# Kernel optimization log

Hardware: AMD Instinct MI355X
Metric: run time of the kernel (lower is better)

The kernel has to match this reference:

```python
import jax, jax.numpy as jnp
import numpy as np


def _cdist(a, b):
    # Euclidean pairwise distances, [N, M]
    d2 = (jnp.sum(a * a, axis=1)[:, None]
          + jnp.sum(b * b, axis=1)[None, :]
          - 2.0 * (a @ b.T))
    return jnp.sqrt(jnp.maximum(d2, 0.0))


def setup_inputs() -> dict:
    key = jax.random.key(0)
    k1, k2 = jax.random.split(key)
    N, M, D = 12288, 12288, 3
    true_pos = jax.random.normal(k1, (N, D), dtype=jnp.float32)
    pred_pos = jax.random.normal(k2, (M, D), dtype=jnp.float32)
    return {"true_pos": true_pos, "pred_pos": pred_pos}


def reference(true_pos, pred_pos):
    dists = _cdist(true_pos.astype(jnp.float32), pred_pos.astype(jnp.float32))
    mins = jnp.min(dists, axis=1)        # per true point -> nearest pred
    mins_seeds = jnp.min(dists, axis=0)  # per pred point -> nearest true
    loss = jnp.mean(mins)
    loss_seeds = jnp.mean(mins_seeds)
    just_in_case_losses = (loss, loss_seeds)
    # use_loss=True branch
    return (loss + loss_seeds, mins_seeds, just_in_case_losses)
```

## Files before the change

### kernel.cpp

```cpp
#include <hip/hip_runtime.h>
#include <cfloat>

typedef __bf16 bf16x8 __attribute__((ext_vector_type(8)));
typedef unsigned short ushort8 __attribute__((ext_vector_type(8)));
typedef float f32x16 __attribute__((ext_vector_type(16)));

#define S_SLICES 4

static __device__ __forceinline__ unsigned short f2bf(float x) {
    unsigned u = __float_as_uint(x);
    return (unsigned short)((u + 0x7FFFu + ((u >> 16) & 1u)) >> 16);
}
static __device__ __forceinline__ float bfbits2f(unsigned short h) {
    return __uint_as_float(((unsigned)h) << 16);
}

__global__ __launch_bounds__(256) void prep_kernel(
    const float* __restrict__ A, const float* __restrict__ B,
    ushort8* __restrict__ RFA, ushort8* __restrict__ CFA,
    ushort8* __restrict__ RFB, ushort8* __restrict__ CFB,
    float* __restrict__ hdr, int n, int m, int RTn, int RTm)
{
    const int i = blockIdx.x * 256 + threadIdx.x;
    if (i < 8) hdr[i] = 0.f;
    const unsigned short one = 0x3F80;

#pragma unroll
    for (int side = 0; side < 2; ++side) {
        const int cntPts = side ? RTm * 32 : RTn * 32;
        if (i >= cntPts) continue;
        const float* P = side ? B : A;
        const int lim = side ? m : n;
        ushort8* RF = side ? RFB : RFA;
        ushort8* CF = side ? CFB : CFA;

        float x = 0.f, y = 0.f, z = 0.f, nrm = 1e30f;
        if (i < lim) { x = P[3*i]; y = P[3*i+1]; z = P[3*i+2];
                       nrm = fmaf(x, x, fmaf(y, y, z * z)); }
        const unsigned short hx = f2bf(x), hy = f2bf(y), hz = f2bf(z);
        const unsigned short lx = f2bf(x - bfbits2f(hx)),
                             ly = f2bf(y - bfbits2f(hy)),
                             lz = f2bf(z - bfbits2f(hz));
        const unsigned short nhx = f2bf(-2.f * bfbits2f(hx)),
                             nhy = f2bf(-2.f * bfbits2f(hy)),
                             nhz = f2bf(-2.f * bfbits2f(hz));
        const unsigned short nlx = f2bf(-2.f * bfbits2f(lx)),
                             nly = f2bf(-2.f * bfbits2f(ly)),
                             nlz = f2bf(-2.f * bfbits2f(lz));
        float r = nrm;
        const unsigned short s1 = f2bf(r); r -= bfbits2f(s1);
        const unsigned short s2 = f2bf(r); r -= bfbits2f(s2);
        const unsigned short s3 = f2bf(r);

        const int t = i >> 5, l5 = i & 31;
        ushort8 rq0 = { nhx, nhy, nhz, nhx, nhy, nhz, nlx, nly };
        ushort8 rq1 = { nlz, s1, s2, s3, one, one, one, 0 };
        RF[t * 64 + l5]      = rq0;
        RF[t * 64 + 32 + l5] = rq1;
        ushort8 cq0 = { hx, hy, hz, lx, ly, lz, hx, hy };
        ushort8 cq1 = { hz, one, one, one, s1, s2, s3, 0 };
        CF[t * 64 + l5]      = cq0;
        CF[t * 64 + 32 + l5] = cq1;
    }
}

#define MINC(C)                                             \
    _Pragma("unroll")                                       \
    for (int r = 0; r < 16; ++r) macc[r] = fminf(macc[r], (C)[r]);

__global__ __launch_bounds__(256, 4) void pairmin_kernel(
    const bf16x8* __restrict__ RFA, const bf16x8* __restrict__ CFA,
    const bf16x8* __restrict__ RFB, const bf16x8* __restrict__ CFB,
    float* __restrict__ sbuf, int RTn, int RTm)
{
    const int lane = threadIdx.x & 63;
    const int wave = threadIdx.x >> 6;

    const bf16x8* RF; const bf16x8* CF; float* sb; int rtCount, ctCount, stride;
    if (blockIdx.z == 0) { RF = RFA; CF = CFB; rtCount = RTn; ctCount = RTm;
                           sb = sbuf; stride = RTn * 32; }
    else                 { RF = RFB; CF = CFA; rtCount = RTm; ctCount = RTn;
                           sb = sbuf + (size_t)S_SLICES * RTn * 32;
                           stride = RTm * 32; }

    const int rt = blockIdx.x * 4 + wave;
    if (rt >= rtCount) return;
    sb += (size_t)blockIdx.y * stride;

    const int ctPer = (ctCount + S_SLICES - 1) / S_SLICES;
    const int ctBeg = min(blockIdx.y * ctPer, ctCount);
    const int ctEnd = min(ctBeg + ctPer, ctCount);

    const bf16x8 afrag = RF[rt * 64 + lane];
    const f32x16 zc = {};

    float macc[16];
#pragma unroll
    for (int r = 0; r < 16; ++r) macc[r] = FLT_MAX;

    if (ctBeg < ctEnd) {
        int ct = ctBeg;
        const int last = ctEnd - 1;
        bf16x8 q0 = CF[(size_t)ct * 64 + lane];
        bf16x8 q1 = CF[(size_t)min(ct + 1, last) * 64 + lane];
        bf16x8 q2 = CF[(size_t)min(ct + 2, last) * 64 + lane];
        bf16x8 q3 = CF[(size_t)min(ct + 3, last) * 64 + lane];
        f32x16 C0 = __builtin_amdgcn_mfma_f32_32x32x16_bf16(afrag, q0, zc, 0, 0, 0);
        f32x16 C1 = __builtin_amdgcn_mfma_f32_32x32x16_bf16(afrag, q1, zc, 0, 0, 0);

        for (; ct + 7 < ctEnd; ct += 4) {
            q0 = CF[(size_t)(ct + 4) * 64 + lane];
            MINC(C0);
            C0 = __builtin_amdgcn_mfma_f32_32x32x16_bf16(afrag, q2, zc, 0, 0, 0);
            q1 = CF[(size_t)(ct + 5) * 64 + lane];
            MINC(C1);
            C1 = __builtin_amdgcn_mfma_f32_32x32x16_bf16(afrag, q3, zc, 0, 0, 0);
            q2 = CF[(size_t)(ct + 6) * 64 + lane];
            MINC(C0);
            C0 = __builtin_amdgcn_mfma_f32_32x32x16_bf16(afrag, q0, zc, 0, 0, 0);
            q3 = CF[(size_t)(ct + 7) * 64 + lane];
            MINC(C1);
            C1 = __builtin_amdgcn_mfma_f32_32x32x16_bf16(afrag, q1, zc, 0, 0, 0);
        }
        MINC(C0);
        MINC(C1);
        if (ct + 2 < ctEnd) {
            const f32x16 C =
                __builtin_amdgcn_mfma_f32_32x32x16_bf16(afrag, q2, zc, 0, 0, 0);
            MINC(C);
        }
        if (ct + 3 < ctEnd) {
            const f32x16 C =
                __builtin_amdgcn_mfma_f32_32x32x16_bf16(afrag, q3, zc, 0, 0, 0);
            MINC(C);
        }
        for (int t = ct + 4; t < ctEnd; ++t) {
            const bf16x8 b = CF[(size_t)t * 64 + lane];
            const f32x16 C =
                __builtin_amdgcn_mfma_f32_32x32x16_bf16(afrag, b, zc, 0, 0, 0);
            MINC(C);
        }
    }

#pragma unroll
    for (int r = 0; r < 16; ++r) {
        float v = macc[r];
        v = fminf(v, __shfl_xor(v, 1, 64));
        v = fminf(v, __shfl_xor(v, 2, 64));
        v = fminf(v, __shfl_xor(v, 4, 64));
        v = fminf(v, __shfl_xor(v, 8, 64));
        v = fminf(v, __shfl_xor(v, 16, 64));
        macc[r] = v;
    }
    if ((lane & 31) == 0) {
        const int q4 = (lane >> 5) * 4;
        float* dst = sb + rt * 32;
#pragma unroll
        for (int r = 0; r < 16; ++r)
            dst[(r & 3) + 8 * (r >> 2) + q4] = macc[r];
    }
}

__global__ __launch_bounds__(256) void finalize_kernel(
    const float* __restrict__ sbuf, float* __restrict__ hdr,
    float* __restrict__ out, int n, int m, int RTn, int RTm)
{
    const int i = blockIdx.x * 256 + threadIdx.x;
    const int strideA = RTn * 32, strideB = RTm * 32;
    const float* sbB = sbuf + (size_t)S_SLICES * strideA;

    float sa = 0.f, sb_ = 0.f;
    if (i < n) {
        float s = FLT_MAX;
#pragma unroll
        for (int k = 0; k < S_SLICES; ++k) s = fminf(s, sbuf[(size_t)k * strideA + i]);
        sa = sqrtf(fmaxf(s, 0.f));
    }
    if (i < m) {
        float s = FLT_MAX;
#pragma unroll
        for (int k = 0; k < S_SLICES; ++k) s = fminf(s, sbB[(size_t)k * strideB + i]);
        const float v = sqrtf(fmaxf(s, 0.f));
        out[1 + i] = v;
        sb_ = v;
    }

#pragma unroll
    for (int off = 32; off > 0; off >>= 1) {
        sa  += __shfl_down(sa,  off, 64);
        sb_ += __shfl_down(sb_, off, 64);
    }
    __shared__ float reda[4], redb[4];
    const int wave = threadIdx.x >> 6;
    const int lane = threadIdx.x & 63;
    if (lane == 0) { reda[wave] = sa; redb[wave] = sb_; }
    __syncthreads();

    if (threadIdx.x == 0) {
        const float ta = reda[0] + reda[1] + reda[2] + reda[3];
        const float tb = redb[0] + redb[1] + redb[2] + redb[3];
        atomicAdd(&hdr[0], ta);
        atomicAdd(&hdr[1], tb);
        __threadfence();
        const unsigned ticket = atomicAdd((unsigned*)&hdr[2], 1u);
        if (ticket == (unsigned)(gridDim.x - 1)) {
            const float fa = atomicAdd(&hdr[0], 0.f);
            const float fb = atomicAdd(&hdr[1], 0.f);
            const float loss = fa / (float)n;
            const float loss_seeds = fb / (float)m;
            out[0] = loss + loss_seeds;
            out[1 + m] = loss;
            out[2 + m] = loss_seeds;
        }
    }
}

extern "C" void kernel_launch(void* const* d_in, const int* in_sizes, int n_in,
                              void* d_out, int out_size, void* d_ws, size_t ws_size,
                              hipStream_t stream) {
    const int n = in_sizes[0] / 3;
    const int m = in_sizes[1] / 3;
    const float* A = (const float*)d_in[0];
    const float* B = (const float*)d_in[1];
    float* out = (float*)d_out;

    const int RTn = (n + 31) / 32, RTm = (m + 31) / 32;
    char* p = (char*)d_ws;
    float*   hdr  = (float*)p;    p += 64;
    float*   sbuf = (float*)p;    p += (size_t)S_SLICES * (RTn + RTm) * 32 * 4;
    ushort8* RFA  = (ushort8*)p;  p += (size_t)RTn * 64 * 16;
    ushort8* CFA  = (ushort8*)p;  p += (size_t)RTn * 64 * 16;
    ushort8* RFB  = (ushort8*)p;  p += (size_t)RTm * 64 * 16;
    ushort8* CFB  = (ushort8*)p;

    const int maxPts = ((RTn > RTm) ? RTn : RTm) * 32;
    prep_kernel<<<(maxPts + 255) / 256, 256, 0, stream>>>(
        A, B, RFA, CFA, RFB, CFB, hdr, n, m, RTn, RTm);

    const int maxRT = (RTn > RTm) ? RTn : RTm;
    dim3 grid((maxRT + 3) / 4, S_SLICES, 2);
    pairmin_kernel<<<grid, 256, 0, stream>>>(
        (const bf16x8*)RFA, (const bf16x8*)CFA,
        (const bf16x8*)RFB, (const bf16x8*)CFB, sbuf, RTn, RTm);

    const int maxnm = (n > m) ? n : m;
    finalize_kernel<<<(maxnm + 255) / 256, 256, 0, stream>>>(
        sbuf, hdr, out, n, m, RTn, RTm);
}
```

Before: 78.16 us.

## Fuse finalize into pairmin via per-row-tile last-slice ticket reduction

Removes the separate finalize kernel. Each wave bumps a per-row-tile atomic counter after writing its partial minima, and the last of the S_SLICES waves to arrive combines the slices, takes the sqrt, writes the outputs and adds to the global sums. A global ticket then lets the final tile write the loss scalars. This saves one kernel launch and an extra pass over sbuf, in exchange for extra atomics and threadfences in every wave plus counter zeroing in prep.

New measurement: 138.9 us. 1.78x slower.

```diff
diff --git a/kernel.cpp b/kernel.cpp
--- a/kernel.cpp
+++ b/kernel.cpp
@@ -19,10 +19,13 @@
     const float* __restrict__ A, const float* __restrict__ B,
     ushort8* __restrict__ RFA, ushort8* __restrict__ CFA,
     ushort8* __restrict__ RFB, ushort8* __restrict__ CFB,
-    float* __restrict__ hdr, int n, int m, int RTn, int RTm)
+    float* __restrict__ hdr, unsigned* __restrict__ rtc,
+    int n, int m, int RTn, int RTm)
 {
     const int i = blockIdx.x * 256 + threadIdx.x;
     if (i < 8) hdr[i] = 0.f;
+    const int maxRT = (RTn > RTm) ? RTn : RTm;
+    if (i < 2 * maxRT) rtc[i] = 0u;
     const unsigned short one = 0x3F80;
 
 #pragma unroll
@@ -71,21 +74,25 @@
 __global__ __launch_bounds__(256, 4) void pairmin_kernel(
     const bf16x8* __restrict__ RFA, const bf16x8* __restrict__ CFA,
     const bf16x8* __restrict__ RFB, const bf16x8* __restrict__ CFB,
-    float* __restrict__ sbuf, int RTn, int RTm)
+    float* __restrict__ sbuf, unsigned* __restrict__ rtc,
+    float* __restrict__ hdr, float* __restrict__ out,
+    int n, int m, int RTn, int RTm)
 {
     const int lane = threadIdx.x & 63;
     const int wave = threadIdx.x >> 6;
-
-    const bf16x8* RF; const bf16x8* CF; float* sb; int rtCount, ctCount, stride;
+    const int maxRT = (RTn > RTm) ? RTn : RTm;
+
+    const bf16x8* RF; const bf16x8* CF; float* sb0;
+    int rtCount, ctCount, stride, lim;
     if (blockIdx.z == 0) { RF = RFA; CF = CFB; rtCount = RTn; ctCount = RTm;
-                           sb = sbuf; stride = RTn * 32; }
+                           sb0 = sbuf; stride = RTn * 32; lim = n; }
     else                 { RF = RFB; CF = CFA; rtCount = RTm; ctCount = RTn;
-                           sb = sbuf + (size_t)S_SLICES * RTn * 32;
-                           stride = RTm * 32; }
+                           sb0 = sbuf + (size_t)S_SLICES * RTn * 32;
+                           stride = RTm * 32; lim = m; }
 
     const int rt = blockIdx.x * 4 + wave;
     if (rt >= rtCount) return;
-    sb += (size_t)blockIdx.y * stride;
+    float* sby = sb0 + (size_t)blockIdx.y * stride;
 
     const int ctPer = (ctCount + S_SLICES - 1) / S_SLICES;
     const int ctBeg = min(blockIdx.y * ctPer, ctCount);
@@ -154,63 +161,47 @@
     }
     if ((lane & 31) == 0) {
         const int q4 = (lane >> 5) * 4;
-        float* dst = sb + rt * 32;
+        float* dst = sby + rt * 32;
 #pragma unroll
         for (int r = 0; r < 16; ++r)
             dst[(r & 3) + 8 * (r >> 2) + q4] = macc[r];
     }
-}
-
-__global__ __launch_bounds__(256) void finalize_kernel(
-    const float* __restrict__ sbuf, float* __restrict__ hdr,
-    float* __restrict__ out, int n, int m, int RTn, int RTm)
-{
-    const int i = blockIdx.x * 256 + threadIdx.x;
-    const int strideA = RTn * 32, strideB = RTm * 32;
-    const float* sbB = sbuf + (size_t)S_SLICES * strideA;
-
-    float sa = 0.f, sb_ = 0.f;
-    if (i < n) {
-        float s = FLT_MAX;
-#pragma unroll
-        for (int k = 0; k < S_SLICES; ++k) s = fminf(s, sbuf[(size_t)k * strideA + i]);
-        sa = sqrtf(fmaxf(s, 0.f));
-    }
-    if (i < m) {
-        float s = FLT_MAX;
-#pragma unroll
-        for (int k = 0; k < S_SLICES; ++k) s = fminf(s, sbB[(size_t)k * strideB + i]);
-        const float v = sqrtf(fmaxf(s, 0.f));
-        out[1 + i] = v;
-        sb_ = v;
-    }
-
-#pragma unroll
-    for (int off = 32; off > 0; off >>= 1) {
-        sa  += __shfl_down(sa,  off, 64);
-        sb_ += __shfl_down(sb_, off, 64);
-    }
-    __shared__ float reda[4], redb[4];
-    const int wave = threadIdx.x >> 6;
-    const int lane = threadIdx.x & 63;
-    if (lane == 0) { reda[wave] = sa; redb[wave] = sb_; }
-    __syncthreads();
-
-    if (threadIdx.x == 0) {
-        const float ta = reda[0] + reda[1] + reda[2] + reda[3];
-        const float tb = redb[0] + redb[1] + redb[2] + redb[3];
-        atomicAdd(&hdr[0], ta);
-        atomicAdd(&hdr[1], tb);
+
+    unsigned tk = 0u;
+    if (lane == 0) {
         __threadfence();
-        const unsigned ticket = atomicAdd((unsigned*)&hdr[2], 1u);
-        if (ticket == (unsigned)(gridDim.x - 1)) {
-            const float fa = atomicAdd(&hdr[0], 0.f);
-            const float fb = atomicAdd(&hdr[1], 0.f);
-            const float loss = fa / (float)n;
-            const float loss_seeds = fb / (float)m;
-            out[0] = loss + loss_seeds;
-            out[1 + m] = loss;
-            out[2 + m] = loss_seeds;
+        tk = atomicAdd(&rtc[blockIdx.z * maxRT + rt], 1u);
+    }
+    tk = __shfl(tk, 0, 64);
+    if (tk == S_SLICES - 1) {
+        const int idx = rt * 32 + (lane & 31);
+        float d = 0.f;
+        if (lane < 32) {
+            float s = FLT_MAX;
+#pragma unroll
+            for (int k = 0; k < S_SLICES; ++k)
+                s = fminf(s, sb0[(size_t)k * stride + idx]);
+            if (idx < lim) {
+                d = sqrtf(fmaxf(s, 0.f));
+                if (blockIdx.z == 1) out[1 + idx] = d;
+            }
+        }
+#pragma unroll
+        for (int off = 32; off > 0; off >>= 1)
+            d += __shfl_down(d, off, 64);
+        if (lane == 0) {
+            atomicAdd(&hdr[blockIdx.z], d);
+            __threadfence();
+            const unsigned g = atomicAdd((unsigned*)&hdr[2], 1u);
+            if (g == (unsigned)(RTn + RTm - 1)) {
+                const float fa = atomicAdd(&hdr[0], 0.f);
+                const float fb = atomicAdd(&hdr[1], 0.f);
+                const float loss = fa / (float)n;
+                const float loss_seeds = fb / (float)m;
+                out[0] = loss + loss_seeds;
+                out[1 + m] = loss;
+                out[2 + m] = loss_seeds;
+            }
         }
     }
 }
@@ -225,25 +216,23 @@
     float* out = (float*)d_out;
 
     const int RTn = (n + 31) / 32, RTm = (m + 31) / 32;
+    const int maxRT = (RTn > RTm) ? RTn : RTm;
     char* p = (char*)d_ws;
-    float*   hdr  = (float*)p;    p += 64;
-    float*   sbuf = (float*)p;    p += (size_t)S_SLICES * (RTn + RTm) * 32 * 4;
-    ushort8* RFA  = (ushort8*)p;  p += (size_t)RTn * 64 * 16;
-    ushort8* CFA  = (ushort8*)p;  p += (size_t)RTn * 64 * 16;
-    ushort8* RFB  = (ushort8*)p;  p += (size_t)RTm * 64 * 16;
-    ushort8* CFB  = (ushort8*)p;
-
-    const int maxPts = ((RTn > RTm) ? RTn : RTm) * 32;
+    float*    hdr  = (float*)p;    p += 64;
+    unsigned* rtc  = (unsigned*)p; p += (((size_t)2 * maxRT * 4 + 63) / 64) * 64;
+    float*    sbuf = (float*)p;    p += (size_t)S_SLICES * (RTn + RTm) * 32 * 4;
+    ushort8*  RFA  = (ushort8*)p;  p += (size_t)RTn * 64 * 16;
+    ushort8*  CFA  = (ushort8*)p;  p += (size_t)RTn * 64 * 16;
+    ushort8*  RFB  = (ushort8*)p;  p += (size_t)RTm * 64 * 16;
+    ushort8*  CFB  = (ushort8*)p;
+
+    const int maxPts = maxRT * 32;
     prep_kernel<<<(maxPts + 255) / 256, 256, 0, stream>>>(
-        A, B, RFA, CFA, RFB, CFB, hdr, n, m, RTn, RTm);
-
-    const int maxRT = (RTn > RTm) ? RTn : RTm;
+        A, B, RFA, CFA, RFB, CFB, hdr, rtc, n, m, RTn, RTm);
+
     dim3 grid((maxRT + 3) / 4, S_SLICES, 2);
     pairmin_kernel<<<grid, 256, 0, stream>>>(
         (const bf16x8*)RFA, (const bf16x8*)CFA,
-        (const bf16x8*)RFB, (const bf16x8*)CFB, sbuf, RTn, RTm);
-
-    const int maxnm = (n > m) ? n : m;
-    finalize_kernel<<<(maxnm + 255) / 256, 256, 0, stream>>>(
-        sbuf, hdr, out, n, m, RTn, RTm);
-}
+        (const bf16x8*)RFB, (const bf16x8*)CFB,
+        sbuf, rtc, hdr, out, n, m, RTn, RTm);
+}
```

## Process two row tiles per wave to reuse column fragments and double slices

Applied to the files above, without the earlier changes.

Each wave now computes two 32-row tiles against every loaded column fragment, so each global load of CF feeds two MFMAs, halving column-fragment traffic per output. Min reduction is fused as a three-way fminf across two column tiles. To keep enough waves in flight after halving the row-wave count, the column dimension is split into 8 slices instead of 4, and launch bounds are relaxed to 3 blocks per CU to accommodate doubled accumulator registers. Risks include register pressure, lower occupancy and more partial results for finalize to combine.

Result: slower. 87.50 us (+11.9%).

```diff
diff --git a/kernel.cpp b/kernel.cpp
--- a/kernel.cpp
+++ b/kernel.cpp
@@ -5,7 +5,7 @@
 typedef unsigned short ushort8 __attribute__((ext_vector_type(8)));
 typedef float f32x16 __attribute__((ext_vector_type(16)));
 
-#define S_SLICES 4
+#define S_SLICES 8
 
 static __device__ __forceinline__ unsigned short f2bf(float x) {
     unsigned u = __float_as_uint(x);
@@ -64,11 +64,15 @@
     }
 }
 
-#define MINC(C)                                             \
+#define MINC(M, C)                                          \
     _Pragma("unroll")                                       \
-    for (int r = 0; r < 16; ++r) macc[r] = fminf(macc[r], (C)[r]);
-
-__global__ __launch_bounds__(256, 4) void pairmin_kernel(
+    for (int r = 0; r < 16; ++r) M[r] = fminf(M[r], (C)[r]);
+#define MIN3(M, Ca, Cb)                                     \
+    _Pragma("unroll")                                       \
+    for (int r = 0; r < 16; ++r)                            \
+        M[r] = fminf(M[r], fminf((Ca)[r], (Cb)[r]));
+
+__global__ __launch_bounds__(256, 3) void pairmin_kernel(
     const bf16x8* __restrict__ RFA, const bf16x8* __restrict__ CFA,
     const bf16x8* __restrict__ RFB, const bf16x8* __restrict__ CFB,
     float* __restrict__ sbuf, int RTn, int RTm)
@@ -83,20 +87,24 @@
                            sb = sbuf + (size_t)S_SLICES * RTn * 32;
                            stride = RTm * 32; }
 
-    const int rt = blockIdx.x * 4 + wave;
-    if (rt >= rtCount) return;
+    const int pairCount = (rtCount + 1) >> 1;
+    const int g = blockIdx.x * 4 + wave;
+    if (g >= pairCount) return;
+    const int rt0 = g * 2;
+    const int rt1 = min(rt0 + 1, rtCount - 1);
     sb += (size_t)blockIdx.y * stride;
 
     const int ctPer = (ctCount + S_SLICES - 1) / S_SLICES;
-    const int ctBeg = min(blockIdx.y * ctPer, ctCount);
+    const int ctBeg = min((int)blockIdx.y * ctPer, ctCount);
     const int ctEnd = min(ctBeg + ctPer, ctCount);
 
-    const bf16x8 afrag = RF[rt * 64 + lane];
+    const bf16x8 a0 = RF[rt0 * 64 + lane];
+    const bf16x8 a1 = RF[rt1 * 64 + lane];
     const f32x16 zc = {};
 
-    float macc[16];
-#pragma unroll
-    for (int r = 0; r < 16; ++r) macc[r] = FLT_MAX;
+    float macc0[16], macc1[16];
+#pragma unroll
+    for (int r = 0; r < 16; ++r) { macc0[r] = FLT_MAX; macc1[r] = FLT_MAX; }
 
     if (ctBeg < ctEnd) {
         int ct = ctBeg;
@@ -105,59 +113,83 @@
         bf16x8 q1 = CF[(size_t)min(ct + 1, last) * 64 + lane];
         bf16x8 q2 = CF[(size_t)min(ct + 2, last) * 64 + lane];
         bf16x8 q3 = CF[(size_t)min(ct + 3, last) * 64 + lane];
-        f32x16 C0 = __builtin_amdgcn_mfma_f32_32x32x16_bf16(afrag, q0, zc, 0, 0, 0);
-        f32x16 C1 = __builtin_amdgcn_mfma_f32_32x32x16_bf16(afrag, q1, zc, 0, 0, 0);
+        f32x16 C00 = __builtin_amdgcn_mfma_f32_32x32x16_bf16(a0, q0, zc, 0, 0, 0);
+        f32x16 C10 = __builtin_amdgcn_mfma_f32_32x32x16_bf16(a1, q0, zc, 0, 0, 0);
+        f32x16 C01 = __builtin_amdgcn_mfma_f32_32x32x16_bf16(a0, q1, zc, 0, 0, 0);
+        f32x16 C11 = __builtin_amdgcn_mfma_f32_32x32x16_bf16(a1, q1, zc, 0, 0, 0);
 
         for (; ct + 7 < ctEnd; ct += 4) {
             q0 = CF[(size_t)(ct + 4) * 64 + lane];
-            MINC(C0);
-            C0 = __builtin_amdgcn_mfma_f32_32x32x16_bf16(afrag, q2, zc, 0, 0, 0);
             q1 = CF[(size_t)(ct + 5) * 64 + lane];
-            MINC(C1);
-            C1 = __builtin_amdgcn_mfma_f32_32x32x16_bf16(afrag, q3, zc, 0, 0, 0);
+            MIN3(macc0, C00, C01);
+            MIN3(macc1, C10, C11);
+            C00 = __builtin_amdgcn_mfma_f32_32x32x16_bf16(a0, q2, zc, 0, 0, 0);
+            C10 = __builtin_amdgcn_mfma_f32_32x32x16_bf16(a1, q2, zc, 0, 0, 0);
+            C01 = __builtin_amdgcn_mfma_f32_32x32x16_bf16(a0, q3, zc, 0, 0, 0);
+            C11 = __builtin_amdgcn_mfma_f32_32x32x16_bf16(a1, q3, zc, 0, 0, 0);
             q2 = CF[(size_t)(ct + 6) * 64 + lane];
-            MINC(C0);
-            C0 = __builtin_amdgcn_mfma_f32_32x32x16_bf16(afrag, q0, zc, 0, 0, 0);
             q3 = CF[(size_t)(ct + 7) * 64 + lane];
-            MINC(C1);
-            C1 = __builtin_amdgcn_mfma_f32_32x32x16_bf16(afrag, q1, zc, 0, 0, 0);
-        }
-        MINC(C0);
-        MINC(C1);
+            MIN3(macc0, C00, C01);
+            MIN3(macc1, C10, C11);
+            C00 = __builtin_amdgcn_mfma_f32_32x32x16_bf16(a0, q0, zc, 0, 0, 0);
+            C10 = __builtin_amdgcn_mfma_f32_32x32x16_bf16(a1, q0, zc, 0, 0, 0);
+            C01 = __builtin_amdgcn_mfma_f32_32x32x16_bf16(a0, q1, zc, 0, 0, 0);
+            C11 = __builtin_amdgcn_mfma_f32_32x32x16_bf16(a1, q1, zc, 0, 0, 0);
+        }
+        MIN3(macc0, C00, C01);
+        MIN3(macc1, C10, C11);
         if (ct + 2 < ctEnd) {
-            const f32x16 C =
-                __builtin_amdgcn_mfma_f32_32x32x16_bf16(afrag, q2, zc, 0, 0, 0);
-            MINC(C);
+            const f32x16 c0 =
+                __builtin_amdgcn_mfma_f32_32x32x16_bf16(a0, q2, zc, 0, 0, 0);
+            const f32x16 c1 =
+                __builtin_amdgcn_mfma_f32_32x32x16_bf16(a1, q2, zc, 0, 0, 0);
+            MINC(macc0, c0);
+            MINC(macc1, c1);
         }
         if (ct + 3 < ctEnd) {
-            const f32x16 C =
-                __builtin_amdgcn_mfma_f32_32x32x16_bf16(afrag, q3, zc, 0, 0, 0);
-            MINC(C);
+            const f32x16 c0 =
+                __builtin_amdgcn_mfma_f32_32x32x16_bf16(a0, q3, zc, 0, 0, 0);
+            const f32x16 c1 =
+                __builtin_amdgcn_mfma_f32_32x32x16_bf16(a1, q3, zc, 0, 0, 0);
+            MINC(macc0, c0);
+            MINC(macc1, c1);
         }
         for (int t = ct + 4; t < ctEnd; ++t) {
             const bf16x8 b = CF[(size_t)t * 64 + lane];
-            const f32x16 C =
-                __builtin_amdgcn_mfma_f32_32x32x16_bf16(afrag, b, zc, 0, 0, 0);
-            MINC(C);
+            const f32x16 c0 =
+                __builtin_amdgcn_mfma_f32_32x32x16_bf16(a0, b, zc, 0, 0, 0);
+            const f32x16 c1 =
+                __builtin_amdgcn_mfma_f32_32x32x16_bf16(a1, b, zc, 0, 0, 0);
+            MINC(macc0, c0);
+            MINC(macc1, c1);
         }
     }
 
 #pragma unroll
     for (int r = 0; r < 16; ++r) {
-        float v = macc[r];
-        v = fminf(v, __shfl_xor(v, 1, 64));
-        v = fminf(v, __shfl_xor(v, 2, 64));
-        v = fminf(v, __shfl_xor(v, 4, 64));
-        v = fminf(v, __shfl_xor(v, 8, 64));
-        v = fminf(v, __shfl_xor(v, 16, 64));
-        macc[r] = v;
+        float v0 = macc0[r], v1 = macc1[r];
+        v0 = fminf(v0, __shfl_xor(v0, 1, 64));
+        v1 = fminf(v1, __shfl_xor(v1, 1, 64));
+        v0 = fminf(v0, __shfl_xor(v0, 2, 64));
+        v1 = fminf(v1, __shfl_xor(v1, 2, 64));
+        v0 = fminf(v0, __shfl_xor(v0, 4, 64));
+        v1 = fminf(v1, __shfl_xor(v1, 4, 64));
+        v0 = fminf(v0, __shfl_xor(v0, 8, 64));
+        v1 = fminf(v1, __shfl_xor(v1, 8, 64));
+        v0 = fminf(v0, __shfl_xor(v0, 16, 64));
+        v1 = fminf(v1, __shfl_xor(v1, 16, 64));
+        macc0[r] = v0;
+        macc1[r] = v1;
     }
     if ((lane & 31) == 0) {
         const int q4 = (lane >> 5) * 4;
-        float* dst = sb + rt * 32;
-#pragma unroll
-        for (int r = 0; r < 16; ++r)
-            dst[(r & 3) + 8 * (r >> 2) + q4] = macc[r];
+        float* dst0 = sb + rt0 * 32;
+        float* dst1 = sb + rt1 * 32;
+#pragma unroll
+        for (int r = 0; r < 16; ++r) {
+            dst0[(r & 3) + 8 * (r >> 2) + q4] = macc0[r];
+            dst1[(r & 3) + 8 * (r >> 2) + q4] = macc1[r];
+        }
     }
 }
 
@@ -233,12 +265,13 @@
     ushort8* RFB  = (ushort8*)p;  p += (size_t)RTm * 64 * 16;
     ushort8* CFB  = (ushort8*)p;
 
-    const int maxPts = ((RTn > RTm) ? RTn : RTm) * 32;
+    const int maxRT = (RTn > RTm) ? RTn : RTm;
+    const int maxPts = maxRT * 32;
     prep_kernel<<<(maxPts + 255) / 256, 256, 0, stream>>>(
         A, B, RFA, CFA, RFB, CFB, hdr, n, m, RTn, RTm);
 
-    const int maxRT = (RTn > RTm) ? RTn : RTm;
-    dim3 grid((maxRT + 3) / 4, S_SLICES, 2);
+    const int maxPair = (maxRT + 1) >> 1;
+    dim3 grid((maxPair + 3) / 4, S_SLICES, 2);
     pairmin_kernel<<<grid, 256, 0, stream>>>(
         (const bf16x8*)RFA, (const bf16x8*)CFA,
         (const bf16x8*)RFB, (const bf16x8*)CFB, sbuf, RTn, RTm);
```

## Stage column fragments in LDS via global_load_lds shared across waves

Applied to the files above, without the earlier changes.

Each block now cooperatively copies chunks of 48 column tiles into shared memory with direct global-to-LDS loads, and all four waves read their B fragments from LDS instead of each wave loading them separately from global memory. The aim is to cut redundant global/L2 traffic, since all four waves in a block use the same column tiles. The inner loop is also reordered to issue MFMA pairs and fold two results per min pass. Occupancy is lowered to 3 blocks per SM and block-wide barriers are added, and out-of-range waves now stay alive to join the barriers.

Result: slower. 86.55 us (+10.7%).

```diff
diff --git a/kernel.cpp b/kernel.cpp
--- a/kernel.cpp
+++ b/kernel.cpp
@@ -6,6 +6,7 @@
 typedef float f32x16 __attribute__((ext_vector_type(16)));
 
 #define S_SLICES 4
+#define CHUNK_T 48
 
 static __device__ __forceinline__ unsigned short f2bf(float x) {
     unsigned u = __float_as_uint(x);
@@ -67,8 +68,12 @@
 #define MINC(C)                                             \
     _Pragma("unroll")                                       \
     for (int r = 0; r < 16; ++r) macc[r] = fminf(macc[r], (C)[r]);
-
-__global__ __launch_bounds__(256, 4) void pairmin_kernel(
+#define MIN3(Ca, Cb)                                        \
+    _Pragma("unroll")                                       \
+    for (int r = 0; r < 16; ++r)                            \
+        macc[r] = fminf(macc[r], fminf((Ca)[r], (Cb)[r]));
+
+__global__ __launch_bounds__(256, 3) void pairmin_kernel(
     const bf16x8* __restrict__ RFA, const bf16x8* __restrict__ CFA,
     const bf16x8* __restrict__ RFB, const bf16x8* __restrict__ CFB,
     float* __restrict__ sbuf, int RTn, int RTm)
@@ -84,58 +89,72 @@
                            stride = RTm * 32; }
 
     const int rt = blockIdx.x * 4 + wave;
-    if (rt >= rtCount) return;
+    const bool live = rt < rtCount;
+    const int rtc = live ? rt : rtCount - 1;
     sb += (size_t)blockIdx.y * stride;
 
     const int ctPer = (ctCount + S_SLICES - 1) / S_SLICES;
-    const int ctBeg = min(blockIdx.y * ctPer, ctCount);
+    const int ctBeg = min((int)blockIdx.y * ctPer, ctCount);
     const int ctEnd = min(ctBeg + ctPer, ctCount);
 
-    const bf16x8 afrag = RF[rt * 64 + lane];
+    const bf16x8 afrag = RF[rtc * 64 + lane];
     const f32x16 zc = {};
 
     float macc[16];
 #pragma unroll
     for (int r = 0; r < 16; ++r) macc[r] = FLT_MAX;
 
-    if (ctBeg < ctEnd) {
-        int ct = ctBeg;
-        const int last = ctEnd - 1;
-        bf16x8 q0 = CF[(size_t)ct * 64 + lane];
-        bf16x8 q1 = CF[(size_t)min(ct + 1, last) * 64 + lane];
-        bf16x8 q2 = CF[(size_t)min(ct + 2, last) * 64 + lane];
-        bf16x8 q3 = CF[(size_t)min(ct + 3, last) * 64 + lane];
-        f32x16 C0 = __builtin_amdgcn_mfma_f32_32x32x16_bf16(afrag, q0, zc, 0, 0, 0);
-        f32x16 C1 = __builtin_amdgcn_mfma_f32_32x32x16_bf16(afrag, q1, zc, 0, 0, 0);
-
-        for (; ct + 7 < ctEnd; ct += 4) {
-            q0 = CF[(size_t)(ct + 4) * 64 + lane];
-            MINC(C0);
+    __shared__ __align__(16) char ldsbuf[CHUNK_T * 1024];
+    const bf16x8* L = (const bf16x8*)ldsbuf;
+    const char* CFb = (const char*)CF;
+
+    for (int cb = ctBeg; cb < ctEnd; cb += CHUNK_T) {
+        const int T = min(CHUNK_T, ctEnd - cb);
+        const int Tbytes = T << 10;
+
+        __syncthreads();
+        const size_t gb = ((size_t)cb) << 10;
+        const int nr = (Tbytes + 4095) >> 12;
+        for (int r = 0; r < nr; ++r) {
+            const int off = (r << 12) + (wave << 10) + (lane << 4);
+            if (off < Tbytes)
+                __builtin_amdgcn_global_load_lds(
+                    (const __attribute__((address_space(1))) void*)(CFb + gb + off),
+                    (__attribute__((address_space(3))) void*)(ldsbuf + (r << 12) + (wave << 10)),
+                    16, 0, 0);
+        }
+        __syncthreads();
+
+        int t0 = 0;
+        if (T >= 4) {
+            bf16x8 q0 = L[0 * 64 + lane];
+            bf16x8 q1 = L[1 * 64 + lane];
+            bf16x8 q2 = L[2 * 64 + lane];
+            bf16x8 q3 = L[3 * 64 + lane];
+            f32x16 C0 = __builtin_amdgcn_mfma_f32_32x32x16_bf16(afrag, q0, zc, 0, 0, 0);
+            f32x16 C1 = __builtin_amdgcn_mfma_f32_32x32x16_bf16(afrag, q1, zc, 0, 0, 0);
+
+            int t = 0;
+            for (; t + 7 < T; t += 4) {
+                q0 = L[(t + 4) * 64 + lane];
+                q1 = L[(t + 5) * 64 + lane];
+                MIN3(C0, C1);
+                C0 = __builtin_amdgcn_mfma_f32_32x32x16_bf16(afrag, q2, zc, 0, 0, 0);
+                C1 = __builtin_amdgcn_mfma_f32_32x32x16_bf16(afrag, q3, zc, 0, 0, 0);
+                q2 = L[(t + 6) * 64 + lane];
+                q3 = L[(t + 7) * 64 + lane];
+                MIN3(C0, C1);
+                C0 = __builtin_amdgcn_mfma_f32_32x32x16_bf16(afrag, q0, zc, 0, 0, 0);
+                C1 = __builtin_amdgcn_mfma_f32_32x32x16_bf16(afrag, q1, zc, 0, 0, 0);
+            }
+            MIN3(C0, C1);
             C0 = __builtin_amdgcn_mfma_f32_32x32x16_bf16(afrag, q2, zc, 0, 0, 0);
-            q1 = CF[(size_t)(ct + 5) * 64 + lane];
-            MINC(C1);
             C1 = __builtin_amdgcn_mfma_f32_32x32x16_bf16(afrag, q3, zc, 0, 0, 0);
-            q2 = CF[(size_t)(ct + 6) * 64 + lane];
-            MINC(C0);
-            C0 = __builtin_amdgcn_mfma_f32_32x32x16_bf16(afrag, q0, zc, 0, 0, 0);
-            q3 = CF[(size_t)(ct + 7) * 64 + lane];
-            MINC(C1);
-            C1 = __builtin_amdgcn_mfma_f32_32x32x16_bf16(afrag, q1, zc, 0, 0, 0);
-        }
-        MINC(C0);
-        MINC(C1);
-        if (ct + 2 < ctEnd) {
-            const f32x16 C =
-                __builtin_amdgcn_mfma_f32_32x32x16_bf16(afrag, q2, zc, 0, 0, 0);
-            MINC(C);
-        }
-        if (ct + 3 < ctEnd) {
-            const f32x16 C =
-                __builtin_amdgcn_mfma_f32_32x32x16_bf16(afrag, q3, zc, 0, 0, 0);
-            MINC(C);
-        }
-        for (int t = ct + 4; t < ctEnd; ++t) {
-            const bf16x8 b = CF[(size_t)t * 64 + lane];
+            MIN3(C0, C1);
+            t0 = t + 4;
+        }
+        for (int u = t0; u < T; ++u) {
+            const bf16x8 b = L[u * 64 + lane];
             const f32x16 C =
                 __builtin_amdgcn_mfma_f32_32x32x16_bf16(afrag, b, zc, 0, 0, 0);
             MINC(C);
@@ -152,7 +171,7 @@
         v = fminf(v, __shfl_xor(v, 16, 64));
         macc[r] = v;
     }
-    if ((lane & 31) == 0) {
+    if (live && (lane & 31) == 0) {
         const int q4 = (lane >> 5) * 4;
         float* dst = sb + rt * 32;
 #pragma unroll
@@ -233,11 +252,11 @@
     ushort8* RFB  = (ushort8*)p;  p += (size_t)RTm * 64 * 16;
     ushort8* CFB  = (ushort8*)p;
 
-    const int maxPts = ((RTn > RTm) ? RTn : RTm) * 32;
+    const int maxRT = (RTn > RTm) ? RTn : RTm;
+    const int maxPts = maxRT * 32;
     prep_kernel<<<(maxPts + 255) / 256, 256, 0, stream>>>(
         A, B, RFA, CFA, RFB, CFB, hdr, n, m, RTn, RTm);
 
-    const int maxRT = (RTn > RTm) ? RTn : RTm;
     dim3 grid((maxRT + 3) / 4, S_SLICES, 2);
     pairmin_kernel<<<grid, 256, 0, stream>>>(
         (const bf16x8*)RFA, (const bf16x8*)CFA,
```
